# Kernel optimization log

Measured on AMD Instinct MI355X. Metric: run time of the kernel, lower is better.

The kernel has to match this reference:

```python
import jax, jax.numpy as jnp
import numpy as np

# --- constants matching init_kwargs / defaults in the torch module ---
N_HID = 1024
N_INP = 1
DT = 0.05
RHO = 0.99
INPUT_SCALING = 1.0
GAMMA_RANGE = (2.0, 3.0)
EPS_RANGE = (0.5, 1.5)
THETA = 0.1        # spike threshold (default arg of cell)
TAU_MEM = 20.0     # LI filter time constant (default arg of forward_li_features)
FADING = False


def setup_inputs() -> dict:
    key = jax.random.key(0)
    B, T = 128, 500
    x = jax.random.normal(key, (B, T, N_INP), dtype=jnp.float32)

    rng = np.random.default_rng(0)
    # h2h = 2*(2*rand-1), then spectral_norm_scaling to spectral radius rho
    h2h = 2.0 * (2.0 * rng.random((N_HID, N_HID)) - 1.0)
    cur_rho = np.max(np.abs(np.linalg.eigvals(h2h)))
    h2h = (h2h * (RHO / cur_rho)).astype(np.float32)
    x2h = (rng.random((N_INP, N_HID)) * INPUT_SCALING).astype(np.float32)
    bias = ((rng.random(N_HID) * 2.0 - 1.0) * INPUT_SCALING).astype(np.float32)
    gamma = (rng.random(N_HID) * (GAMMA_RANGE[1] - GAMMA_RANGE[0]) + GAMMA_RANGE[0]).astype(np.float32)
    epsilon = (rng.random(N_HID) * (EPS_RANGE[1] - EPS_RANGE[0]) + EPS_RANGE[0]).astype(np.float32)

    return {
        "x": x,
        "h2h": jnp.asarray(h2h),
        "x2h": jnp.asarray(x2h),
        "bias": jnp.asarray(bias),
        "gamma": jnp.asarray(gamma),
        "epsilon": jnp.asarray(epsilon),
    }


def reference(x, h2h, x2h, bias, gamma, epsilon):
    B, T, _ = x.shape
    n_hid = h2h.shape[0]
    dt = jnp.float32(DT)
    alpha = jnp.exp(jnp.float32(-1.0 / TAU_MEM))

    def step(carry, xt):
        hy, hz, u, tot = carry
        # coupled-oscillator cell (ref_period stays identically zero in the source)
        pre = jnp.tanh(xt @ x2h + hy @ h2h + bias)       # (B, n_hid)
        hz = hz + dt * (pre - gamma * hy - epsilon * hz)
        if FADING:
            hz = hz - dt * hz
        hy = hy + dt * hz
        if FADING:
            hy = hy - dt * hy
        s = (hy - THETA > 0).astype(jnp.float32)          # spike
        u = u * alpha + s * (1.0 - alpha)                 # LI filter
        tot = tot + s.sum()
        return (hy, hz, u, tot), None

    z = jnp.zeros((B, n_hid), dtype=jnp.float32)
    init = (z, z, z, jnp.float32(0.0))
    xs = jnp.swapaxes(x, 0, 1)                            # (T, B, n_inp)
    (hy, hz, u, tot), _ = jax.lax.scan(step, init, xs)
    avg_firing_rate = tot / (B * T * n_hid)
    return u, avg_firing_rate
```

## Files before the change

kernel.cpp:

```cpp
#include <hip/hip_runtime.h>
#include <math.h>

typedef unsigned long long u64;
typedef unsigned int u32;

#define N_HID   1024
#define NBATCH  128
#define TSTEPS  500
#define DT      0.05f
#define THETA   0.1f

#define B_WG   8
#define C_WG   64
#define KSPL   8
#define KSEG   (N_HID / KSPL)
#define NGRP   (NBATCH / B_WG)
#define NCT    (N_HID / C_WG)
#define NWG    (NGRP * NCT)

#define CTRL_TOT    0
#define CTRL_GRP    64
#define CTRL_WORDS  (CTRL_GRP + NGRP * 64)

__device__ __forceinline__ u32 a_ld32(const u32* p) {
    return __hip_atomic_load(p, __ATOMIC_RELAXED, __HIP_MEMORY_SCOPE_AGENT);
}
__device__ __forceinline__ void a_st32(u32* p, u32 v) {
    __hip_atomic_store(p, v, __ATOMIC_RELAXED, __HIP_MEMORY_SCOPE_AGENT);
}
__device__ __forceinline__ u64 a_ld64(const u64* p) {
    return __hip_atomic_load(p, __ATOMIC_RELAXED, __HIP_MEMORY_SCOPE_AGENT);
}
__device__ __forceinline__ void a_st64(u64* p, u64 v) {
    __hip_atomic_store(p, v, __ATOMIC_RELAXED, __HIP_MEMORY_SCOPE_AGENT);
}

#define FMA16(hv, wv4) do { \
    acc[0][0]=fmaf((hv).x,(wv4).x,acc[0][0]); acc[0][1]=fmaf((hv).x,(wv4).y,acc[0][1]); \
    acc[0][2]=fmaf((hv).x,(wv4).z,acc[0][2]); acc[0][3]=fmaf((hv).x,(wv4).w,acc[0][3]); \
    acc[1][0]=fmaf((hv).y,(wv4).x,acc[1][0]); acc[1][1]=fmaf((hv).y,(wv4).y,acc[1][1]); \
    acc[1][2]=fmaf((hv).y,(wv4).z,acc[1][2]); acc[1][3]=fmaf((hv).y,(wv4).w,acc[1][3]); \
    acc[2][0]=fmaf((hv).z,(wv4).x,acc[2][0]); acc[2][1]=fmaf((hv).z,(wv4).y,acc[2][1]); \
    acc[2][2]=fmaf((hv).z,(wv4).z,acc[2][2]); acc[2][3]=fmaf((hv).z,(wv4).w,acc[2][3]); \
    acc[3][0]=fmaf((hv).w,(wv4).x,acc[3][0]); acc[3][1]=fmaf((hv).w,(wv4).y,acc[3][1]); \
    acc[3][2]=fmaf((hv).w,(wv4).z,acc[3][2]); acc[3][3]=fmaf((hv).w,(wv4).w,acc[3][3]); \
} while (0)

__global__ __launch_bounds__(256, 1) void persist_kernel(
    const float* __restrict__ x,
    const float* __restrict__ W,
    const float* __restrict__ x2h,
    const float* __restrict__ bias,
    const float* __restrict__ gam,
    const float* __restrict__ eps,
    float* __restrict__ hyT0,
    float* __restrict__ hyT1,
    float* __restrict__ uout,
    u32* __restrict__ ctrl,
    float alpha, float oma)
{
    __shared__ float sh_hyT[2][N_HID * B_WG];
    __shared__ float sh_part[2][KSPL * B_WG * C_WG];
    __shared__ u32 sh_cnt;

    const int tid = threadIdx.x;
    if (tid == 0) sh_cnt = 0u;

    const int bid   = blockIdx.x;
    const int xcd   = bid & 7;
    const int idx   = bid >> 3;
    const int ctile = xcd * 2 + (idx & 1);
    const int btile = idx >> 1;
    const int c0g   = ctile * C_WG;
    const int b0    = btile * B_WG;

    const int cg  = tid & 15;
    const int bg  = (tid >> 4) & 1;
    const int ks  = tid >> 5;
    const int bl0 = bg * 4;
    const int k0  = ks * KSEG;
    const float* Wp = W + (size_t)k0 * N_HID + c0g + cg * 4;

    const int wv   = tid >> 6;
    const int lane = tid & 63;
    u32* flags = ctrl + CTRL_GRP + (btile << 6);
    u32* mypoll = flags + 16 * wv + (lane & 15);
    u32* mypub  = flags + ctile * 4 + wv;

    const int c2  = tid >> 2;
    const int b2  = (tid & 3) * 2;
    const int cgl = c0g + c2;
    const float x2h_c  = x2h[cgl];
    const float bias_c = bias[cgl];
    const float gam_c  = gam[cgl];
    const float eps_c  = eps[cgl];
    const float* xrow0 = x + (size_t)(b0 + b2)     * TSTEPS;
    const float* xrow1 = x + (size_t)(b0 + b2 + 1) * TSTEPS;

    float hz0 = 0.f, hz1 = 0.f, u0 = 0.f, u1 = 0.f;
    u32 spikes = 0;

    for (int t = 0; t < TSTEPS; ++t) {
        const float* src = (t & 1) ? hyT1 : hyT0;
        float*       dst = (t & 1) ? hyT0 : hyT1;
        float* hyt  = sh_hyT[t & 1];
        float* part = sh_part[t & 1];

        const float xa = xrow0[t];
        const float xb = xrow1[t];

        if (t == 0) {
            u64* s64 = (u64*)hyt;
            #pragma unroll
            for (int it = 0; it < 16; ++it)
                s64[(wv << 10) + it * 64 + lane] = 0ull;
        } else {
            while (!__all(a_ld32(mypoll) >= (u32)t))
                __builtin_amdgcn_s_sleep(1);
            u64 tmp[16];
            #pragma unroll
            for (int it = 0; it < 16; ++it) {
                const int i    = it * 64 + lane;
                const int k    = (wv << 8) + (i >> 2);
                const int pair = i & 3;
                const u64* sp = (const u64*)(src + (size_t)k * NBATCH + b0) + pair;
                tmp[it] = a_ld64(sp);
            }
            u64* s64 = (u64*)hyt;
            #pragma unroll
            for (int it = 0; it < 16; ++it)
                s64[(wv << 10) + it * 64 + lane] = tmp[it];
        }

        float acc[4][4];
        #pragma unroll
        for (int i = 0; i < 4; ++i)
            #pragma unroll
            for (int jj = 0; jj < 4; ++jj) acc[i][jj] = 0.f;

        #pragma unroll 8
        for (int kk = 0; kk < KSEG; ++kk) {
            const float4 hv  = *(const float4*)(&hyt[(k0 + kk) * B_WG + bl0]);
            const float4 wv4 = *(const float4*)(Wp + (size_t)kk * N_HID);
            FMA16(hv, wv4);
        }

        #pragma unroll
        for (int bi = 0; bi < 4; ++bi) {
            float4 v = make_float4(acc[bi][0], acc[bi][1], acc[bi][2], acc[bi][3]);
            *(float4*)(&part[((ks * B_WG) + bl0 + bi) * C_WG + cg * 4]) = v;
        }
        __syncthreads();

        float hyn0, hyn1;
        {
            float sum = part[(0 * B_WG + b2) * C_WG + c2];
            #pragma unroll
            for (int s2 = 1; s2 < KSPL; ++s2)
                sum += part[(s2 * B_WG + b2) * C_WG + c2];
            const float pre = tanhf(fmaf(xa, x2h_c, sum) + bias_c);
            const float hyv = hyt[cgl * B_WG + b2];
            hz0 = fmaf(DT, pre - gam_c * hyv - eps_c * hz0, hz0);
            hyn0 = fmaf(DT, hz0, hyv);
            const int s = ((hyn0 - THETA) > 0.f) ? 1 : 0;
            u0 = fmaf(u0, alpha, (float)s * oma);
            spikes += (u32)s;
        }
        {
            float sum = part[(0 * B_WG + b2 + 1) * C_WG + c2];
            #pragma unroll
            for (int s2 = 1; s2 < KSPL; ++s2)
                sum += part[(s2 * B_WG + b2 + 1) * C_WG + c2];
            const float pre = tanhf(fmaf(xb, x2h_c, sum) + bias_c);
            const float hyv = hyt[cgl * B_WG + b2 + 1];
            hz1 = fmaf(DT, pre - gam_c * hyv - eps_c * hz1, hz1);
            hyn1 = fmaf(DT, hz1, hyv);
            const int s = ((hyn1 - THETA) > 0.f) ? 1 : 0;
            u1 = fmaf(u1, alpha, (float)s * oma);
            spikes += (u32)s;
        }
        {
            float2 f2 = make_float2(hyn0, hyn1);
            u64 v;
            __builtin_memcpy(&v, &f2, 8);
            a_st64((u64*)(dst + (size_t)cgl * NBATCH + b0 + b2), v);
        }

        asm volatile("s_waitcnt vmcnt(0)" ::: "memory");
        if (lane == 0) a_st32(mypub, (u32)(t + 1));
    }

    uout[(size_t)(b0 + b2)     * N_HID + cgl] = u0;
    uout[(size_t)(b0 + b2 + 1) * N_HID + cgl] = u1;

    u32 s = spikes;
    s += __shfl_down(s, 32);
    s += __shfl_down(s, 16);
    s += __shfl_down(s, 8);
    s += __shfl_down(s, 4);
    s += __shfl_down(s, 2);
    s += __shfl_down(s, 1);
    if ((tid & 63) == 0) atomicAdd(&sh_cnt, s);
    __syncthreads();
    if (tid == 0) atomicAdd(ctrl + CTRL_TOT, sh_cnt);
}

__global__ void init_kernel(u32* ctrl)
{
    const int i = blockIdx.x * blockDim.x + threadIdx.x;
    if (i < CTRL_WORDS) {
        __hip_atomic_store(ctrl + i, 0u, __ATOMIC_RELAXED,
                           __HIP_MEMORY_SCOPE_AGENT);
    }
}

__global__ void final_kernel(const u32* __restrict__ ctrl,
                             float* __restrict__ out_rate)
{
    if (threadIdx.x == 0 && blockIdx.x == 0) {
        const double denom = (double)NBATCH * (double)TSTEPS * (double)N_HID;
        *out_rate = (float)((double)ctrl[CTRL_TOT] / denom);
    }
}

extern "C" void kernel_launch(void* const* d_in, const int* in_sizes, int n_in,
                              void* d_out, int out_size, void* d_ws, size_t ws_size,
                              hipStream_t stream)
{
    const float* x    = (const float*)d_in[0];
    const float* h2h  = (const float*)d_in[1];
    const float* x2h  = (const float*)d_in[2];
    const float* bias = (const float*)d_in[3];
    const float* gam  = (const float*)d_in[4];
    const float* eps  = (const float*)d_in[5];

    float* out = (float*)d_out;

    float* hyT0 = (float*)d_ws;
    float* hyT1 = hyT0 + (size_t)NBATCH * N_HID;
    u32*   ctrl = (u32*)(hyT1 + (size_t)NBATCH * N_HID);

    init_kernel<<<dim3((CTRL_WORDS + 255) / 256), dim3(256), 0, stream>>>(ctrl);

    float alpha = expf(-1.0f / 20.0f);
    float oma   = 1.0f - alpha;

    void* args[] = {
        (void*)&x, (void*)&h2h, (void*)&x2h, (void*)&bias, (void*)&gam,
        (void*)&eps, (void*)&hyT0, (void*)&hyT1, (void*)&out, (void*)&ctrl,
        (void*)&alpha, (void*)&oma
    };
    hipLaunchCooperativeKernel((const void*)persist_kernel,
                               dim3(NWG), dim3(256), args, 0, stream);

    final_kernel<<<dim3(1), dim3(64), 0, stream>>>(
        ctrl, out + (size_t)NBATCH * N_HID);
}
```

Before: 4.108 ms.

## Split hidden-state gather into two halves overlapped with partial matmul

Each wave now polls the readiness flags for the first half of its K segment, loads and multiplies that half, and only then waits for the second half's producers. This lets compute start before every producer tile has published, cutting the critical-path wait in the persistent step loop. The shared hidden-state buffer is no longer double-buffered, the partial-sum buffer gets a padded stride to avoid bank conflicts, and each thread keeps its own previous hy in registers instead of rereading shared memory. Dropping the double buffer relies on the existing per-step barrier ordering to prevent races between waves.

```diff
diff --git a/kernel.cpp b/kernel.cpp
--- a/kernel.cpp
+++ b/kernel.cpp
@@ -17,6 +17,7 @@
 #define NGRP   (NBATCH / B_WG)
 #define NCT    (N_HID / C_WG)
 #define NWG    (NGRP * NCT)
+#define PLD    68
 
 #define CTRL_TOT    0
 #define CTRL_GRP    64
@@ -59,8 +60,8 @@
     u32* __restrict__ ctrl,
     float alpha, float oma)
 {
-    __shared__ float sh_hyT[2][N_HID * B_WG];
-    __shared__ float sh_part[2][KSPL * B_WG * C_WG];
+    __shared__ float sh_hyT[N_HID * B_WG];
+    __shared__ float sh_part[2][KSPL * B_WG * PLD];
     __shared__ u32 sh_cnt;
 
     const int tid = threadIdx.x;
@@ -84,8 +85,11 @@
     const int wv   = tid >> 6;
     const int lane = tid & 63;
     u32* flags = ctrl + CTRL_GRP + (btile << 6);
-    u32* mypoll = flags + 16 * wv + (lane & 15);
-    u32* mypub  = flags + ctile * 4 + wv;
+    const int pbaseA = ((lane & 4) ? (4 * wv + 2) : (4 * wv)) * 4 + (lane & 3);
+    const int pbaseB = ((lane & 4) ? (4 * wv + 3) : (4 * wv + 1)) * 4 + (lane & 3);
+    u32* mypollA = flags + pbaseA;
+    u32* mypollB = flags + pbaseB;
+    u32* mypub   = flags + ctile * 4 + wv;
 
     const int c2  = tid >> 2;
     const int b2  = (tid & 3) * 2;
@@ -98,39 +102,16 @@
     const float* xrow1 = x + (size_t)(b0 + b2 + 1) * TSTEPS;
 
     float hz0 = 0.f, hz1 = 0.f, u0 = 0.f, u1 = 0.f;
+    float hyp0 = 0.f, hyp1 = 0.f;
     u32 spikes = 0;
 
     for (int t = 0; t < TSTEPS; ++t) {
         const float* src = (t & 1) ? hyT1 : hyT0;
         float*       dst = (t & 1) ? hyT0 : hyT1;
-        float* hyt  = sh_hyT[t & 1];
         float* part = sh_part[t & 1];
 
         const float xa = xrow0[t];
         const float xb = xrow1[t];
-
-        if (t == 0) {
-            u64* s64 = (u64*)hyt;
-            #pragma unroll
-            for (int it = 0; it < 16; ++it)
-                s64[(wv << 10) + it * 64 + lane] = 0ull;
-        } else {
-            while (!__all(a_ld32(mypoll) >= (u32)t))
-                __builtin_amdgcn_s_sleep(1);
-            u64 tmp[16];
-            #pragma unroll
-            for (int it = 0; it < 16; ++it) {
-                const int i    = it * 64 + lane;
-                const int k    = (wv << 8) + (i >> 2);
-                const int pair = i & 3;
-                const u64* sp = (const u64*)(src + (size_t)k * NBATCH + b0) + pair;
-                tmp[it] = a_ld64(sp);
-            }
-            u64* s64 = (u64*)hyt;
-            #pragma unroll
-            for (int it = 0; it < 16; ++it)
-                s64[(wv << 10) + it * 64 + lane] = tmp[it];
-        }
 
         float acc[4][4];
         #pragma unroll
@@ -138,46 +119,117 @@
             #pragma unroll
             for (int jj = 0; jj < 4; ++jj) acc[i][jj] = 0.f;
 
-        #pragma unroll 8
-        for (int kk = 0; kk < KSEG; ++kk) {
-            const float4 hv  = *(const float4*)(&hyt[(k0 + kk) * B_WG + bl0]);
-            const float4 wv4 = *(const float4*)(Wp + (size_t)kk * N_HID);
-            FMA16(hv, wv4);
+        u64* s64 = (u64*)sh_hyT;
+        const u64* src64 = (const u64*)src;
+
+        if (t == 0) {
+            #pragma unroll
+            for (int it = 0; it < 16; ++it)
+                s64[(wv << 10) + it * 64 + lane] = 0ull;
+            asm volatile("" ::: "memory");
+            #pragma unroll 8
+            for (int kk = 0; kk < KSEG; ++kk) {
+                const float4 hv  = *(const float4*)(&sh_hyT[(k0 + kk) * B_WG + bl0]);
+                const float4 wv4 = *(const float4*)(Wp + (size_t)kk * N_HID);
+                FMA16(hv, wv4);
+            }
+        } else {
+            while (!__all(a_ld32(mypollA) >= (u32)t))
+                __builtin_amdgcn_s_sleep(1);
+            {
+                u64 tmp[8];
+                #pragma unroll
+                for (int it = 0; it < 8; ++it) {
+                    const int e     = it * 64 + lane;
+                    const int k_rel = e >> 2;
+                    const int pair  = e & 3;
+                    const int kA    = k_rel + ((k_rel >> 6) << 6);
+                    tmp[it] = a_ld64(src64 + (size_t)((wv << 8) + kA) * 64
+                                     + (b0 >> 1) + pair);
+                }
+                #pragma unroll
+                for (int it = 0; it < 8; ++it) {
+                    const int e     = it * 64 + lane;
+                    const int k_rel = e >> 2;
+                    const int pair  = e & 3;
+                    const int kA    = k_rel + ((k_rel >> 6) << 6);
+                    s64[(wv << 10) + kA * 4 + pair] = tmp[it];
+                }
+            }
+            asm volatile("" ::: "memory");
+            #pragma unroll 8
+            for (int kk = 0; kk < 64; ++kk) {
+                const float4 hv  = *(const float4*)(&sh_hyT[(k0 + kk) * B_WG + bl0]);
+                const float4 wv4 = *(const float4*)(Wp + (size_t)kk * N_HID);
+                FMA16(hv, wv4);
+            }
+            asm volatile("" ::: "memory");
+
+            while (!__all(a_ld32(mypollB) >= (u32)t))
+                __builtin_amdgcn_s_sleep(1);
+            {
+                u64 tmp[8];
+                #pragma unroll
+                for (int it = 0; it < 8; ++it) {
+                    const int e     = it * 64 + lane;
+                    const int k_rel = e >> 2;
+                    const int pair  = e & 3;
+                    const int kB    = k_rel + 64 + ((k_rel >> 6) << 6);
+                    tmp[it] = a_ld64(src64 + (size_t)((wv << 8) + kB) * 64
+                                     + (b0 >> 1) + pair);
+                }
+                #pragma unroll
+                for (int it = 0; it < 8; ++it) {
+                    const int e     = it * 64 + lane;
+                    const int k_rel = e >> 2;
+                    const int pair  = e & 3;
+                    const int kB    = k_rel + 64 + ((k_rel >> 6) << 6);
+                    s64[(wv << 10) + kB * 4 + pair] = tmp[it];
+                }
+            }
+            asm volatile("" ::: "memory");
+            #pragma unroll 8
+            for (int kk = 64; kk < KSEG; ++kk) {
+                const float4 hv  = *(const float4*)(&sh_hyT[(k0 + kk) * B_WG + bl0]);
+                const float4 wv4 = *(const float4*)(Wp + (size_t)kk * N_HID);
+                FMA16(hv, wv4);
+            }
+            asm volatile("" ::: "memory");
         }
 
         #pragma unroll
         for (int bi = 0; bi < 4; ++bi) {
             float4 v = make_float4(acc[bi][0], acc[bi][1], acc[bi][2], acc[bi][3]);
-            *(float4*)(&part[((ks * B_WG) + bl0 + bi) * C_WG + cg * 4]) = v;
+            *(float4*)(&part[((ks * B_WG) + bl0 + bi) * PLD + cg * 4]) = v;
         }
         __syncthreads();
 
         float hyn0, hyn1;
         {
-            float sum = part[(0 * B_WG + b2) * C_WG + c2];
+            float sum = part[(0 * B_WG + b2) * PLD + c2];
             #pragma unroll
             for (int s2 = 1; s2 < KSPL; ++s2)
-                sum += part[(s2 * B_WG + b2) * C_WG + c2];
+                sum += part[(s2 * B_WG + b2) * PLD + c2];
             const float pre = tanhf(fmaf(xa, x2h_c, sum) + bias_c);
-            const float hyv = hyt[cgl * B_WG + b2];
-            hz0 = fmaf(DT, pre - gam_c * hyv - eps_c * hz0, hz0);
-            hyn0 = fmaf(DT, hz0, hyv);
+            hz0 = fmaf(DT, pre - gam_c * hyp0 - eps_c * hz0, hz0);
+            hyn0 = fmaf(DT, hz0, hyp0);
             const int s = ((hyn0 - THETA) > 0.f) ? 1 : 0;
             u0 = fmaf(u0, alpha, (float)s * oma);
             spikes += (u32)s;
+            hyp0 = hyn0;
         }
         {
-            float sum = part[(0 * B_WG + b2 + 1) * C_WG + c2];
+            float sum = part[(0 * B_WG + b2 + 1) * PLD + c2];
             #pragma unroll
             for (int s2 = 1; s2 < KSPL; ++s2)
-                sum += part[(s2 * B_WG + b2 + 1) * C_WG + c2];
+                sum += part[(s2 * B_WG + b2 + 1) * PLD + c2];
             const float pre = tanhf(fmaf(xb, x2h_c, sum) + bias_c);
-            const float hyv = hyt[cgl * B_WG + b2 + 1];
-            hz1 = fmaf(DT, pre - gam_c * hyv - eps_c * hz1, hz1);
-            hyn1 = fmaf(DT, hz1, hyv);
+            hz1 = fmaf(DT, pre - gam_c * hyp1 - eps_c * hz1, hz1);
+            hyn1 = fmaf(DT, hz1, hyp1);
             const int s = ((hyn1 - THETA) > 0.f) ? 1 : 0;
             u1 = fmaf(u1, alpha, (float)s * oma);
             spikes += (u32)s;
+            hyp1 = hyn1;
         }
         {
             float2 f2 = make_float2(hyn0, hyn1);
```

After: 4.176 ms. Within noise of the previous version (+1.7%).
